# Kernel optimization log

Hardware: AMD Instinct MI355X
Metric: run time of the kernel (lower is better)

Reference implementation:

```python
import jax, jax.numpy as jnp
import numpy as np

N_NODES = 100000
N_EDGES = 3200000
NFEAT, NHID, NOUT = 256, 128, 64


def spmm(edge_row, edge_col, edge_val, dense):
    # out[r] = sum_{e: row[e]==r} val[e] * dense[col[e]]
    gathered = dense[edge_col] * edge_val[:, None]  # [E, F]
    return jax.ops.segment_sum(gathered, edge_row, num_segments=N_NODES)


def setup_inputs() -> dict:
    key = jax.random.key(0)
    ks = jax.random.split(key, 8)
    stdv1 = 1.0 / np.sqrt(NHID)
    stdv2 = 1.0 / np.sqrt(NOUT)
    return {
        "x": jax.random.normal(ks[0], (N_NODES, NFEAT), dtype=jnp.float32),
        "edge_row": jax.random.randint(ks[1], (N_EDGES,), 0, N_NODES, dtype=jnp.int32),
        "edge_col": jax.random.randint(ks[2], (N_EDGES,), 0, N_NODES, dtype=jnp.int32),
        "edge_val": jax.random.uniform(ks[3], (N_EDGES,), dtype=jnp.float32),
        "W1": jax.random.uniform(ks[4], (NFEAT, NHID), jnp.float32, -stdv1, stdv1),
        "b1": jax.random.uniform(ks[5], (NHID,), jnp.float32, -stdv1, stdv1),
        "W2": jax.random.uniform(ks[6], (NHID, NOUT), jnp.float32, -stdv2, stdv2),
        "b2": jax.random.uniform(ks[7], (NOUT,), jnp.float32, -stdv2, stdv2),
    }


def reference(x, edge_row, edge_col, edge_val, W1, b1, W2, b2):
    # layer 1: dense projection, SpMM aggregate, bias, ReLU
    support = x @ W1                                   # [N, NHID]
    h = spmm(edge_row, edge_col, edge_val, support) + b1
    h = jax.nn.relu(h)
    # dropout skipped (eval mode: training=False)
    # layer 2
    support2 = h @ W2                                  # [N, NOUT]
    out = spmm(edge_row, edge_col, edge_val, support2) + b2
    return out
```

## Files before the change

### kernel.cpp

```cpp
#include <hip/hip_runtime.h>
#include <hip/hip_bf16.h>

#define N_NODES 100000
#define N_EDGES 3200000
#define NFEAT 256
#define NHID 128
#define NOUT 64

#define BSHIFT 8
#define BROWS 256
#define NBUCK 391
#define EPB 4096
#define NBLK1 ((N_EDGES + EPB - 1) / EPB)

typedef __attribute__((ext_vector_type(8))) short short8;
typedef __attribute__((ext_vector_type(8))) unsigned short ushort8_t;
typedef __attribute__((ext_vector_type(4))) float f32x4;

__device__ __forceinline__ unsigned short f2bf(float f) {
    union { float f; unsigned int u; } v; v.f = f;
    unsigned int r = v.u + 0x7fffu + ((v.u >> 16) & 1u);
    return (unsigned short)(r >> 16);
}
__device__ __forceinline__ float bflo(unsigned int u) { return __uint_as_float(u << 16); }
__device__ __forceinline__ float bfhi(unsigned int u) { return __uint_as_float(u & 0xffff0000u); }


__global__ __launch_bounds__(256) void bcount_cvtw(const int* __restrict__ erow,
                                                   int* __restrict__ Mt,
                                                   const float* __restrict__ W1,
                                                   const float* __restrict__ W2,
                                                   unsigned short* __restrict__ W1b,
                                                   unsigned short* __restrict__ W2b) {
    __shared__ int h[NBUCK];
    if (blockIdx.x >= NBLK1) {
        const int i = (blockIdx.x - NBLK1) * 256 + threadIdx.x;
        if (i < NFEAT * NHID) W1b[i] = f2bf(W1[i]);
        if (i < NHID * NOUT)  W2b[i] = f2bf(W2[i]);
        return;
    }
    for (int i = threadIdx.x; i < NBUCK; i += 256) h[i] = 0;
    __syncthreads();
    const int base = blockIdx.x * EPB;
    const int n = min(EPB, N_EDGES - base);
    for (int i = threadIdx.x; i < n; i += 256)
        atomicAdd(&h[erow[base + i] >> BSHIFT], 1);
    __syncthreads();
    for (int b = threadIdx.x; b < NBUCK; b += 256)
        Mt[(size_t)b * NBLK1 + blockIdx.x] = h[b];
}


__global__ __launch_bounds__(256) void colscan_kernel(int* __restrict__ Mt,
                                                      int* __restrict__ btot) {
    const int wv = threadIdx.x >> 6, lane = threadIdx.x & 63;
    const int b = blockIdx.x * 4 + wv;
    if (b >= NBUCK) return;
    int* row = Mt + (size_t)b * NBLK1;
    int carry = 0;
    for (int t = 0; t < NBLK1; t += 64) {
        int i = t + lane;
        int v = (i < NBLK1) ? row[i] : 0;
        int x = v;
        #pragma unroll
        for (int off = 1; off < 64; off <<= 1) {
            int tt = __shfl_up(x, off);
            if (lane >= off) x += tt;
        }
        if (i < NBLK1) row[i] = carry + x - v;
        carry += __shfl(x, 63);
    }
    if (lane == 0) btot[b] = carry;
}


__global__ __launch_bounds__(1024) void bscan_kernel(const int* __restrict__ btot,
                                                     int* __restrict__ bbase) {
    __shared__ int wsum[16];
    const int tid = threadIdx.x;
    const int lane = tid & 63;
    int v = (tid < NBUCK) ? btot[tid] : 0;
    int x = v;
    #pragma unroll
    for (int off = 1; off < 64; off <<= 1) {
        int t = __shfl_up(x, off);
        if (lane >= off) x += t;
    }
    if (lane == 63) wsum[tid >> 6] = x;
    __syncthreads();
    if (tid < 16) {
        int s = wsum[tid];
        #pragma unroll
        for (int off = 1; off < 16; off <<= 1) {
            int t = __shfl_up(s, off);
            if (tid >= off) s += t;
        }
        wsum[tid] = s;
    }
    __syncthreads();
    if (tid >= 64) x += wsum[(tid >> 6) - 1];
    if (tid < NBUCK) bbase[tid] = x - v;
    if (tid == NBUCK - 1) bbase[NBUCK] = x;
}


__global__ __launch_bounds__(256) void binsort_kernel(const int* __restrict__ erow,
                                                      const int* __restrict__ ecol,
                                                      const float* __restrict__ eval,
                                                      const int* __restrict__ Mt,
                                                      const int* __restrict__ btot,
                                                      const int* __restrict__ bbase,
                                                      int2* __restrict__ tmp) {
    __shared__ int2 sc[EPB];
    __shared__ unsigned short sb[EPB];
    __shared__ int hist[NBUCK];
    __shared__ int delta[NBUCK];
    __shared__ int scan_t[4];

    const int blk = blockIdx.x;
    const int tid = threadIdx.x;
    const int base = blk * EPB;
    const int n = min(EPB, N_EDGES - base);

    int v0 = 0, v1 = 0, v2 = 0, v3 = 0;
    int m0 = 0, m1 = 0, m2 = 0, m3 = 0;
    {
        const int i0 = tid * 4;
        #define LOADCNT(k, vk, mk) { \
            int idx = i0 + k; \
            if (idx < NBUCK) { \
                mk = Mt[(size_t)idx * NBLK1 + blk]; \
                int nx = (blk + 1 < NBLK1) ? Mt[(size_t)idx * NBLK1 + blk + 1] : btot[idx]; \
                vk = nx - mk; \
            } }
        LOADCNT(0, v0, m0) LOADCNT(1, v1, m1) LOADCNT(2, v2, m2) LOADCNT(3, v3, m3)
        #undef LOADCNT
    }
    int s4 = v0 + v1 + v2 + v3;
    int xi = s4;
    const int lane = tid & 63;
    #pragma unroll
    for (int off = 1; off < 64; off <<= 1) {
        int t = __shfl_up(xi, off);
        if (lane >= off) xi += t;
    }
    if (lane == 63) scan_t[tid >> 6] = xi;
    __syncthreads();
    if (tid == 0) {
        int run = 0;
        #pragma unroll
        for (int w = 0; w < 4; ++w) { int t = scan_t[w]; scan_t[w] = run; run += t; }
    }
    __syncthreads();
    {
        int e0 = scan_t[tid >> 6] + xi - s4;
        int i0 = tid * 4;
        int ex[4] = {e0, e0 + v0, e0 + v0 + v1, e0 + v0 + v1 + v2};
        int mm[4] = {m0, m1, m2, m3};
        #pragma unroll
        for (int k = 0; k < 4; ++k) {
            int idx = i0 + k;
            if (idx < NBUCK) {
                hist[idx] = ex[k];
                delta[idx] = bbase[idx] + mm[k] - ex[k];
            }
        }
    }
    __syncthreads();

    for (int i = tid; i < n; i += 256) {
        int r = erow[base + i];
        int b = r >> BSHIFT;
        int rl = r & (BROWS - 1);
        int pos = atomicAdd(&hist[b], 1);
        sc[pos] = make_int2((rl << 17) | ecol[base + i], __float_as_int(eval[base + i]));
        sb[pos] = (unsigned short)b;
    }
    __syncthreads();

    for (int i = tid; i < n; i += 256) {
        int b = sb[i];
        tmp[delta[b] + i] = sc[i];
    }
}


__global__ __launch_bounds__(256) void gemm1_kernel(const float* __restrict__ X,
                                                    const unsigned short* __restrict__ Wb,
                                                    unsigned short* __restrict__ Y) {
    __shared__ unsigned short bt[128 * 128];
    const int bid = blockIdx.x;
    const int tid = threadIdx.x;
    const int lane = tid & 63;
    const int w = tid >> 6;
    const int rb = bid * 128 + w * 32;
    const int lr = lane & 15;
    const int kg = lane >> 4;
    const int M = N_NODES;

    f32x4 acc[2][8];
    #pragma unroll
    for (int a = 0; a < 2; ++a)
        #pragma unroll
        for (int nf = 0; nf < 8; ++nf)
            #pragma unroll
            for (int i = 0; i < 4; ++i) acc[a][nf][i] = 0.f;

    for (int ph = 0; ph < 2; ++ph) {
        if (ph) __syncthreads();
        {
            const int nn = tid & 127;
            const int kb = tid >> 7;
            #pragma unroll
            for (int kk0 = 0; kk0 < 64; kk0 += 8) {
                const int kk = kb * 64 + kk0;
                unsigned short p[8];
                #pragma unroll
                for (int i = 0; i < 8; ++i)
                    p[i] = Wb[(size_t)(ph * 128 + kk + i) * NHID + nn];
                unsigned int byte = (unsigned int)nn * 256 + (unsigned int)kk * 2;
                byte ^= (unsigned int)(nn & 7) << 4;
                *(ushort8_t*)((char*)bt + byte) = *(const ushort8_t*)p;
            }
        }
        __syncthreads();

        #pragma unroll
        for (int ks = 0; ks < 4; ++ks) {
            const int k0 = ph * 128 + ks * 32 + kg * 8;
            short8 a0, a1;
            #pragma unroll
            for (int af = 0; af < 2; ++af) {
                const int row = rb + af * 16 + lr;
                short8 r;
                if (row < M) {
                    const float* p = X + (size_t)row * NFEAT + k0;
                    float4 u0 = *(const float4*)p;
                    float4 u1 = *(const float4*)(p + 4);
                    unsigned short q[8] = {f2bf(u0.x), f2bf(u0.y), f2bf(u0.z), f2bf(u0.w),
                                           f2bf(u1.x), f2bf(u1.y), f2bf(u1.z), f2bf(u1.w)};
                    r = *(const short8*)q;
                } else {
                    #pragma unroll
                    for (int i = 0; i < 8; ++i) r[i] = 0;
                }
                if (af == 0) a0 = r; else a1 = r;
            }
            #pragma unroll
            for (int nf = 0; nf < 8; ++nf) {
                const int nn = nf * 16 + lr;
                unsigned int byte = (unsigned int)nn * 256 + (unsigned int)(ks * 32 + kg * 8) * 2;
                byte ^= (unsigned int)(nn & 7) << 4;
                short8 bfr = *(const short8*)((const char*)bt + byte);
                acc[0][nf] = __builtin_amdgcn_mfma_f32_16x16x32_bf16(a0, bfr, acc[0][nf], 0, 0, 0);
                acc[1][nf] = __builtin_amdgcn_mfma_f32_16x16x32_bf16(a1, bfr, acc[1][nf], 0, 0, 0);
            }
        }
    }

    #pragma unroll
    for (int af = 0; af < 2; ++af)
        #pragma unroll
        for (int nf = 0; nf < 8; ++nf)
            #pragma unroll
            for (int i = 0; i < 4; ++i) {
                const int r = rb + af * 16 + kg * 4 + i;
                if (r < M) Y[(size_t)r * NHID + nf * 16 + lr] = f2bf(acc[af][nf][i]);
            }
}


__global__ __launch_bounds__(256) void rowsort_kernel(const int* __restrict__ bbase,
                                                      const int2* __restrict__ tmp,
                                                      int2* __restrict__ ec2,
                                                      int* __restrict__ rowptr) {
    __shared__ int h[BROWS];
    __shared__ int hx[BROWS];
    __shared__ int wq[4];

    const int b = blockIdx.x;
    const int s = bbase[b], e = bbase[b + 1];
    const int n = e - s;
    const int tid = threadIdx.x;
    const int lane = tid & 63;

    h[tid] = 0;
    __syncthreads();
    for (int i = tid; i < n; i += 256)
        atomicAdd(&h[((unsigned)tmp[s + i].x) >> 17], 1);
    __syncthreads();

    int v = h[tid];
    int x = v;
    #pragma unroll
    for (int off = 1; off < 64; off <<= 1) {
        int t = __shfl_up(x, off);
        if (lane >= off) x += t;
    }
    if (lane == 63) wq[tid >> 6] = x;
    __syncthreads();
    if (tid == 0) {
        int run = 0;
        #pragma unroll
        for (int w = 0; w < 4; ++w) { int t = wq[w]; wq[w] = run; run += t; }
    }
    __syncthreads();
    x += wq[tid >> 6];
    {
        const int grow = b * BROWS + tid;
        if (grow < N_NODES) rowptr[grow + 1] = s + x;
        if (b == 0 && tid == 0) rowptr[0] = 0;
        hx[tid] = s + (x - v);
    }
    __syncthreads();

    for (int i = tid; i < n; i += 256) {
        int2 d = tmp[s + i];
        unsigned int rl = ((unsigned)d.x) >> 17;
        int pos = atomicAdd(&hx[rl], 1);
        ec2[pos] = make_int2(d.x & 0x1FFFF, d.y);
    }
}


template<int N, int K>
__global__ __launch_bounds__(256) void gemm_mfma(const unsigned short* __restrict__ X,
                                                 const unsigned short* __restrict__ Wb,
                                                 unsigned short* __restrict__ Y, int M) {
    __shared__ unsigned short bt[N * K];
    const int tid = threadIdx.x;

    {
        const int n = tid & (N - 1);
        const int kb = tid / N;
        const int kspan = K / (256 / N);
        for (int k0 = kb * kspan; k0 < (kb + 1) * kspan; k0 += 8) {
            unsigned short p[8];
            #pragma unroll
            for (int i = 0; i < 8; ++i) p[i] = Wb[(size_t)(k0 + i) * N + n];
            unsigned int byte = (unsigned int)n * (K * 2) + (unsigned int)k0 * 2;
            byte ^= (unsigned int)(n & 7) << 4;
            *(ushort8_t*)((char*)bt + byte) = *(const ushort8_t*)p;
        }
    }
    __syncthreads();

    const int lane = tid & 63;
    const int w = tid >> 6;
    const int rb = blockIdx.x * 128 + w * 32;
    const int lr = lane & 15;
    const int kg = lane >> 4;
    constexpr int NF = N / 16;
    constexpr int KS = K / 32;

    f32x4 acc[2][NF];
    #pragma unroll
    for (int a = 0; a < 2; ++a)
        #pragma unroll
        for (int nf = 0; nf < NF; ++nf)
            #pragma unroll
            for (int i = 0; i < 4; ++i) acc[a][nf][i] = 0.f;

    auto loadA = [&](int af, int ks) -> short8 {
        const int row = rb + af * 16 + lr;
        const int k0 = ks * 32 + kg * 8;
        short8 r;
        if (row < M) {
            r = *(const short8*)(X + (size_t)row * K + k0);
        } else {
            #pragma unroll
            for (int i = 0; i < 8; ++i) r[i] = 0;
        }
        return r;
    };
    auto loadB = [&](int nf, int ks) -> short8 {
        const int n = nf * 16 + lr;
        unsigned int byte = (unsigned int)n * (K * 2) + (unsigned int)(ks * 32 + kg * 8) * 2;
        byte ^= (unsigned int)(n & 7) << 4;
        return *(const short8*)((const char*)bt + byte);
    };

    #pragma unroll
    for (int ks = 0; ks < KS; ++ks) {
        short8 a0 = loadA(0, ks), a1 = loadA(1, ks);
        #pragma unroll
        for (int nf = 0; nf < NF; ++nf) {
            short8 bfr = loadB(nf, ks);
            acc[0][nf] = __builtin_amdgcn_mfma_f32_16x16x32_bf16(a0, bfr, acc[0][nf], 0, 0, 0);
            acc[1][nf] = __builtin_amdgcn_mfma_f32_16x16x32_bf16(a1, bfr, acc[1][nf], 0, 0, 0);
        }
    }

    #pragma unroll
    for (int af = 0; af < 2; ++af)
        #pragma unroll
        for (int nf = 0; nf < NF; ++nf)
            #pragma unroll
            for (int i = 0; i < 4; ++i) {
                const int r = rb + af * 16 + kg * 4 + i;
                if (r < M) Y[(size_t)r * N + nf * 16 + lr] = f2bf(acc[af][nf][i]);
            }
}


__global__ __launch_bounds__(256) void spmm1_kernel(const int* __restrict__ rp,
                                                    const int2* __restrict__ ec,
                                                    const unsigned int* __restrict__ d32,
                                                    const float* __restrict__ bias,
                                                    unsigned short* __restrict__ out) {
    const int lane = threadIdx.x & 63;
    const int row = blockIdx.x * 4 + (threadIdx.x >> 6);
    if (row >= N_NODES) return;
    const int s = __builtin_amdgcn_readfirstlane(rp[row]);
    const int e = __builtin_amdgcn_readfirstlane(rp[row + 1]);
    float a0 = 0.f, a1 = 0.f, b0 = 0.f, b1 = 0.f;
    float c0a = 0.f, c1a = 0.f, d0a = 0.f, d1a = 0.f;
    int j = s;
    for (; j + 16 <= e; j += 16) {
        int2 q0 = ec[j],      q1 = ec[j + 1],  q2 = ec[j + 2],  q3 = ec[j + 3];
        int2 q4 = ec[j + 4],  q5 = ec[j + 5],  q6 = ec[j + 6],  q7 = ec[j + 7];
        int2 q8 = ec[j + 8],  q9 = ec[j + 9],  qa = ec[j + 10], qb = ec[j + 11];
        int2 qc = ec[j + 12], qd = ec[j + 13], qe = ec[j + 14], qf = ec[j + 15];
        unsigned int u0 = d32[(size_t)q0.x * 64 + lane];
        unsigned int u1 = d32[(size_t)q1.x * 64 + lane];
        unsigned int u2 = d32[(size_t)q2.x * 64 + lane];
        unsigned int u3 = d32[(size_t)q3.x * 64 + lane];
        unsigned int u4 = d32[(size_t)q4.x * 64 + lane];
        unsigned int u5 = d32[(size_t)q5.x * 64 + lane];
        unsigned int u6 = d32[(size_t)q6.x * 64 + lane];
        unsigned int u7 = d32[(size_t)q7.x * 64 + lane];
        unsigned int u8 = d32[(size_t)q8.x * 64 + lane];
        unsigned int u9 = d32[(size_t)q9.x * 64 + lane];
        unsigned int ua = d32[(size_t)qa.x * 64 + lane];
        unsigned int ub = d32[(size_t)qb.x * 64 + lane];
        unsigned int uc = d32[(size_t)qc.x * 64 + lane];
        unsigned int ud = d32[(size_t)qd.x * 64 + lane];
        unsigned int ue = d32[(size_t)qe.x * 64 + lane];
        unsigned int uf = d32[(size_t)qf.x * 64 + lane];
        float v0 = __int_as_float(q0.y), v1 = __int_as_float(q1.y);
        float v2 = __int_as_float(q2.y), v3 = __int_as_float(q3.y);
        float v4 = __int_as_float(q4.y), v5 = __int_as_float(q5.y);
        float v6 = __int_as_float(q6.y), v7 = __int_as_float(q7.y);
        float v8 = __int_as_float(q8.y), v9 = __int_as_float(q9.y);
        float va = __int_as_float(qa.y), vb = __int_as_float(qb.y);
        float vc = __int_as_float(qc.y), vd = __int_as_float(qd.y);
        float ve = __int_as_float(qe.y), vf = __int_as_float(qf.y);
        a0 += v0 * bflo(u0); a1 += v0 * bfhi(u0);
        b0 += v1 * bflo(u1); b1 += v1 * bfhi(u1);
        c0a += v2 * bflo(u2); c1a += v2 * bfhi(u2);
        d0a += v3 * bflo(u3); d1a += v3 * bfhi(u3);
        a0 += v4 * bflo(u4); a1 += v4 * bfhi(u4);
        b0 += v5 * bflo(u5); b1 += v5 * bfhi(u5);
        c0a += v6 * bflo(u6); c1a += v6 * bfhi(u6);
        d0a += v7 * bflo(u7); d1a += v7 * bfhi(u7);
        a0 += v8 * bflo(u8); a1 += v8 * bfhi(u8);
        b0 += v9 * bflo(u9); b1 += v9 * bfhi(u9);
        c0a += va * bflo(ua); c1a += va * bfhi(ua);
        d0a += vb * bflo(ub); d1a += vb * bfhi(ub);
        a0 += vc * bflo(uc); a1 += vc * bfhi(uc);
        b0 += vd * bflo(ud); b1 += vd * bfhi(ud);
        c0a += ve * bflo(ue); c1a += ve * bfhi(ue);
        d0a += vf * bflo(uf); d1a += vf * bfhi(uf);
    }
    for (; j + 8 <= e; j += 8) {
        int2 q0 = ec[j],     q1 = ec[j + 1], q2 = ec[j + 2], q3 = ec[j + 3];
        int2 q4 = ec[j + 4], q5 = ec[j + 5], q6 = ec[j + 6], q7 = ec[j + 7];
        unsigned int u0 = d32[(size_t)q0.x * 64 + lane];
        unsigned int u1 = d32[(size_t)q1.x * 64 + lane];
        unsigned int u2 = d32[(size_t)q2.x * 64 + lane];
        unsigned int u3 = d32[(size_t)q3.x * 64 + lane];
        unsigned int u4 = d32[(size_t)q4.x * 64 + lane];
        unsigned int u5 = d32[(size_t)q5.x * 64 + lane];
        unsigned int u6 = d32[(size_t)q6.x * 64 + lane];
        unsigned int u7 = d32[(size_t)q7.x * 64 + lane];
        float v0 = __int_as_float(q0.y), v1 = __int_as_float(q1.y);
        float v2 = __int_as_float(q2.y), v3 = __int_as_float(q3.y);
        float v4 = __int_as_float(q4.y), v5 = __int_as_float(q5.y);
        float v6 = __int_as_float(q6.y), v7 = __int_as_float(q7.y);
        a0 += v0 * bflo(u0); a1 += v0 * bfhi(u0);
        b0 += v1 * bflo(u1); b1 += v1 * bfhi(u1);
        c0a += v2 * bflo(u2); c1a += v2 * bfhi(u2);
        d0a += v3 * bflo(u3); d1a += v3 * bfhi(u3);
        a0 += v4 * bflo(u4); a1 += v4 * bfhi(u4);
        b0 += v5 * bflo(u5); b1 += v5 * bfhi(u5);
        c0a += v6 * bflo(u6); c1a += v6 * bfhi(u6);
        d0a += v7 * bflo(u7); d1a += v7 * bfhi(u7);
    }
    for (; j < e; ++j) {
        int2 c = ec[j];
        float v = __int_as_float(c.y);
        unsigned int u = d32[(size_t)c.x * 64 + lane];
        a0 += v * bflo(u);
        a1 += v * bfhi(u);
    }
    a0 += b0 + c0a + d0a; a1 += b1 + c1a + d1a;
    float2 bp = *(const float2*)(bias + 2 * lane);
    float r0 = fmaxf(a0 + bp.x, 0.f);
    float r1 = fmaxf(a1 + bp.y, 0.f);
    unsigned int pack = (unsigned int)f2bf(r0) | ((unsigned int)f2bf(r1) << 16);
    *(unsigned int*)(out + (size_t)row * 128 + 2 * lane) = pack;
}


__global__ __launch_bounds__(256) void spmm2_kernel(const int* __restrict__ rp,
                                                    const int2* __restrict__ ec,
                                                    const unsigned int* __restrict__ d32,
                                                    const float* __restrict__ bias,
                                                    float* __restrict__ out) {
    const int lane = threadIdx.x & 63;
    const int row = blockIdx.x * 4 + (threadIdx.x >> 6);
    if (row >= N_NODES) return;
    const int s = __builtin_amdgcn_readfirstlane(rp[row]);
    const int e = __builtin_amdgcn_readfirstlane(rp[row + 1]);
    const int eh = lane >> 5, cl = lane & 31;
    float a0 = 0.f, a1 = 0.f, b0 = 0.f, b1 = 0.f;
    float c0a = 0.f, c1a = 0.f, d0a = 0.f, d1a = 0.f;
    int j = s;
    for (; j + 16 <= e; j += 16) {
        int2 q0 = ec[j + eh],      q1 = ec[j + 2 + eh];
        int2 q2 = ec[j + 4 + eh],  q3 = ec[j + 6 + eh];
        int2 q4 = ec[j + 8 + eh],  q5 = ec[j + 10 + eh];
        int2 q6 = ec[j + 12 + eh], q7 = ec[j + 14 + eh];
        unsigned int u0 = d32[(size_t)q0.x * 32 + cl];
        unsigned int u1 = d32[(size_t)q1.x * 32 + cl];
        unsigned int u2 = d32[(size_t)q2.x * 32 + cl];
        unsigned int u3 = d32[(size_t)q3.x * 32 + cl];
        unsigned int u4 = d32[(size_t)q4.x * 32 + cl];
        unsigned int u5 = d32[(size_t)q5.x * 32 + cl];
        unsigned int u6 = d32[(size_t)q6.x * 32 + cl];
        unsigned int u7 = d32[(size_t)q7.x * 32 + cl];
        float v0 = __int_as_float(q0.y), v1 = __int_as_float(q1.y);
        float v2 = __int_as_float(q2.y), v3 = __int_as_float(q3.y);
        float v4 = __int_as_float(q4.y), v5 = __int_as_float(q5.y);
        float v6 = __int_as_float(q6.y), v7 = __int_as_float(q7.y);
        a0 += v0 * bflo(u0); a1 += v0 * bfhi(u0);
        b0 += v1 * bflo(u1); b1 += v1 * bfhi(u1);
        c0a += v2 * bflo(u2); c1a += v2 * bfhi(u2);
        d0a += v3 * bflo(u3); d1a += v3 * bfhi(u3);
        a0 += v4 * bflo(u4); a1 += v4 * bfhi(u4);
        b0 += v5 * bflo(u5); b1 += v5 * bfhi(u5);
        c0a += v6 * bflo(u6); c1a += v6 * bfhi(u6);
        d0a += v7 * bflo(u7); d1a += v7 * bfhi(u7);
    }
    for (; j + 8 <= e; j += 8) {
        int2 q0 = ec[j + eh],     q1 = ec[j + 2 + eh];
        int2 q2 = ec[j + 4 + eh], q3 = ec[j + 6 + eh];
        unsigned int u0 = d32[(size_t)q0.x * 32 + cl];
        unsigned int u1 = d32[(size_t)q1.x * 32 + cl];
        unsigned int u2 = d32[(size_t)q2.x * 32 + cl];
        unsigned int u3 = d32[(size_t)q3.x * 32 + cl];
        float v0 = __int_as_float(q0.y), v1 = __int_as_float(q1.y);
        float v2 = __int_as_float(q2.y), v3 = __int_as_float(q3.y);
        a0 += v0 * bflo(u0); a1 += v0 * bfhi(u0);
        b0 += v1 * bflo(u1); b1 += v1 * bfhi(u1);
        c0a += v2 * bflo(u2); c1a += v2 * bfhi(u2);
        d0a += v3 * bflo(u3); d1a += v3 * bfhi(u3);
    }
    for (; j < e; j += 2) {
        const int j2 = j + eh;
        if (j2 < e) {
            int2 cv = ec[j2];
            float v = __int_as_float(cv.y);
            unsigned int u = d32[(size_t)cv.x * 32 + cl];
            a0 += v * bflo(u);
            a1 += v * bfhi(u);
        }
    }
    a0 += b0 + c0a + d0a; a1 += b1 + c1a + d1a;
    a0 += __shfl_xor(a0, 32);
    a1 += __shfl_xor(a1, 32);
    if (eh == 0) {
        float2 bp = *(const float2*)(bias + 2 * cl);
        *(float2*)(out + (size_t)row * 64 + 2 * cl) = make_float2(a0 + bp.x, a1 + bp.y);
    }
}


extern "C" void kernel_launch(void* const* d_in, const int* in_sizes, int n_in,
                              void* d_out, int out_size, void* d_ws, size_t ws_size,
                              hipStream_t stream) {
    const float* x    = (const float*)d_in[0];
    const int*   erow = (const int*)d_in[1];
    const int*   ecol = (const int*)d_in[2];
    const float* evalv = (const float*)d_in[3];
    const float* W1   = (const float*)d_in[4];
    const float* b1   = (const float*)d_in[5];
    const float* W2   = (const float*)d_in[6];
    const float* b2   = (const float*)d_in[7];
    float* out = (float*)d_out;

    char* wsp = (char*)d_ws;
    size_t off = 0;
    auto alloc = [&](size_t bytes) -> void* {
        void* p = wsp + off;
        off = (off + bytes + 255) & ~(size_t)255;
        return p;
    };
    unsigned short* support = (unsigned short*)alloc((size_t)N_NODES * NHID * 2);
    unsigned short* hbuf    = (unsigned short*)alloc((size_t)N_NODES * NHID * 2);
    int2*  tmp     = (int2*)alloc((size_t)N_EDGES * 8);
    int2*  ec2     = (int2*)alloc((size_t)N_EDGES * 8);
    int*   Mt      = (int*)alloc((size_t)NBUCK * NBLK1 * 4);
    int*   btot    = (int*)alloc((size_t)NBUCK * 4);
    int*   bbase   = (int*)alloc((size_t)(NBUCK + 1) * 4);
    int*   rowptr  = (int*)alloc((size_t)(N_NODES + 1) * 4);
    unsigned short* W1b = (unsigned short*)alloc((size_t)NFEAT * NHID * 2);
    unsigned short* W2b = (unsigned short*)alloc((size_t)NHID * NOUT * 2);

    bcount_cvtw<<<NBLK1 + 128, 256, 0, stream>>>(erow, Mt, W1, W2, W1b, W2b);
    colscan_kernel<<<(NBUCK + 3) / 4, 256, 0, stream>>>(Mt, btot);
    bscan_kernel<<<1, 1024, 0, stream>>>(btot, bbase);
    binsort_kernel<<<NBLK1, 256, 0, stream>>>(erow, ecol, evalv, Mt, btot, bbase, tmp);
    gemm1_kernel<<<(N_NODES + 127) / 128, 256, 0, stream>>>(x, W1b, support);
    rowsort_kernel<<<NBUCK, 256, 0, stream>>>(bbase, tmp, ec2, rowptr);

    spmm1_kernel<<<(N_NODES + 3) / 4, 256, 0, stream>>>(rowptr, ec2, (const unsigned int*)support, b1, hbuf);
    gemm_mfma<NOUT, NHID><<<(N_NODES + 127) / 128, 256, 0, stream>>>(hbuf, W2b, support, N_NODES);
    spmm2_kernel<<<(N_NODES + 3) / 4, 256, 0, stream>>>(rowptr, ec2, (const unsigned int*)support, b2, out);
}
```

Before: 319.0 us.

## Fuse gemm1 and rowsort into one heterogeneous-role kernel launch

```diff
diff --git a/kernel.cpp b/kernel.cpp
--- a/kernel.cpp
+++ b/kernel.cpp
@@ -12,6 +12,7 @@
 #define NBUCK 391
 #define EPB 4096
 #define NBLK1 ((N_EDGES + EPB - 1) / EPB)
+#define GB1 782
 
 typedef __attribute__((ext_vector_type(8))) short short8;
 typedef __attribute__((ext_vector_type(8))) unsigned short ushort8_t;
@@ -185,11 +186,11 @@
 }
 
 
-__global__ __launch_bounds__(256) void gemm1_kernel(const float* __restrict__ X,
-                                                    const unsigned short* __restrict__ Wb,
-                                                    unsigned short* __restrict__ Y) {
-    __shared__ unsigned short bt[128 * 128];
-    const int bid = blockIdx.x;
+__device__ __forceinline__ void gemm1_role(int bid, char* sm,
+                                           const float* __restrict__ X,
+                                           const unsigned short* __restrict__ Wb,
+                                           unsigned short* __restrict__ Y) {
+    unsigned short* bt = (unsigned short*)sm;
     const int tid = threadIdx.x;
     const int lane = tid & 63;
     const int w = tid >> 6;
@@ -269,16 +270,15 @@
             }
 }
 
-
-__global__ __launch_bounds__(256) void rowsort_kernel(const int* __restrict__ bbase,
-                                                      const int2* __restrict__ tmp,
-                                                      int2* __restrict__ ec2,
-                                                      int* __restrict__ rowptr) {
-    __shared__ int h[BROWS];
-    __shared__ int hx[BROWS];
-    __shared__ int wq[4];
-
-    const int b = blockIdx.x;
+__device__ __forceinline__ void rowsort_role(int b, char* sm,
+                                             const int* __restrict__ bbase,
+                                             const int2* __restrict__ tmp,
+                                             int2* __restrict__ ec2,
+                                             int* __restrict__ rowptr) {
+    int* h  = (int*)sm;
+    int* hx = (int*)(sm + 1024);
+    int* wq = (int*)(sm + 2048);
+
     const int s = bbase[b], e = bbase[b + 1];
     const int n = e - s;
     const int tid = threadIdx.x;
@@ -320,6 +320,18 @@
         int pos = atomicAdd(&hx[rl], 1);
         ec2[pos] = make_int2(d.x & 0x1FFFF, d.y);
     }
+}
+
+__global__ __launch_bounds__(256) void rowsort_g1(const int* __restrict__ bbase,
+                                                  const int2* __restrict__ tmp,
+                                                  int2* __restrict__ ec2,
+                                                  int* __restrict__ rowptr,
+                                                  const float* __restrict__ X,
+                                                  const unsigned short* __restrict__ W1b,
+                                                  unsigned short* __restrict__ Y) {
+    extern __shared__ char sm[];
+    if (blockIdx.x < GB1) gemm1_role(blockIdx.x, sm, X, W1b, Y);
+    else                  rowsort_role(blockIdx.x - GB1, sm, bbase, tmp, ec2, rowptr);
 }
 
 
@@ -611,8 +623,8 @@
     colscan_kernel<<<(NBUCK + 3) / 4, 256, 0, stream>>>(Mt, btot);
     bscan_kernel<<<1, 1024, 0, stream>>>(btot, bbase);
     binsort_kernel<<<NBLK1, 256, 0, stream>>>(erow, ecol, evalv, Mt, btot, bbase, tmp);
-    gemm1_kernel<<<(N_NODES + 127) / 128, 256, 0, stream>>>(x, W1b, support);
-    rowsort_kernel<<<NBUCK, 256, 0, stream>>>(bbase, tmp, ec2, rowptr);
+    rowsort_g1<<<GB1 + NBUCK, 256, 32768, stream>>>(bbase, tmp, ec2, rowptr,
+                                                    x, W1b, support);
 
     spmm1_kernel<<<(N_NODES + 3) / 4, 256, 0, stream>>>(rowptr, ec2, (const unsigned int*)support, b1, hbuf);
     gemm_mfma<NOUT, NHID><<<(N_NODES + 127) / 128, 256, 0, stream>>>(hbuf, W2b, support, N_NODES);
```

New measurement: 309.6 us (median of 2 runs). 3.0% less time.
